# Optimization experiments

Measured on AMD Instinct MI355X. Metric: run time of the kernel, lower is better.

Reference implementation:

```python
import jax, jax.numpy as jnp
import numpy as np

N_LAYER = 2


def setup_inputs() -> dict:
    key = jax.random.key(0)
    k1, k2, k3, k4, k5 = jax.random.split(key, 5)
    N, E, D, C = 50000, 800000, 128, 40
    features = jax.random.normal(k1, (N, D), dtype=jnp.float32)
    adj_row = jax.random.randint(k2, (E,), 0, N, dtype=jnp.int32)
    adj_col = jax.random.randint(k3, (E,), 0, N, dtype=jnp.int32)
    adj_values = jax.random.uniform(k4, (E,), dtype=jnp.float32)
    lin = jax.random.normal(k5, (D, C), dtype=jnp.float32) * (1.0 / np.sqrt(D))
    return {"features": features, "adj_row": adj_row, "adj_col": adj_col,
            "adj_values": adj_values, "lin": lin}


def reference(features, adj_row, adj_col, adj_values, lin):
    N = features.shape[0]
    loop = jnp.arange(N, dtype=adj_row.dtype)
    # preprocess_adj: add self-loops, symmetric GCN normalization D^-1/2 (A+I) D^-1/2
    row = jnp.concatenate([adj_row, loop])
    col = jnp.concatenate([adj_col, loop])
    val = jnp.concatenate([adj_values, jnp.ones((N,), features.dtype)])
    deg = jax.ops.segment_sum(val, row, num_segments=N)
    dinv = jnp.where(deg > 0, jax.lax.rsqrt(jnp.maximum(deg, 1e-12)), 0.0)
    nval = dinv[row] * val * dinv[col]  # normalized edge weights [E+N]
    X = features
    layerwise = []
    for _ in range(N_LAYER):  # X = A_hat @ X (SpMM via gather + segment_sum)
        X = jax.ops.segment_sum(nval[:, None] * X[col], row, num_segments=N)
        layerwise.append(X)
    logits = X @ lin  # [N, out_dim]
    return (jax.nn.log_softmax(logits, axis=1), logits, tuple(layerwise))
```

## Files before the change

kernel.cpp:

```cpp
#include <hip/hip_runtime.h>
#include <math.h>

#define D_FEAT 128
#define SCAN_B 256
#define C_MAX  40
#define FIXP   33554432.0f

#define FLAG_AGG (1ull << 32)
#define FLAG_INC (2ull << 32)


__device__ __forceinline__ unsigned bf16_rne(float x) {
    unsigned u = __float_as_uint(x);
    return (u + 0x7fffu + ((u >> 16) & 1u)) >> 16;
}
__device__ __forceinline__ unsigned pack2(float x, float y) {
    return bf16_rne(x) | (bf16_rne(y) << 16);
}
__device__ __forceinline__ float lo_f(unsigned g) { return __uint_as_float(g << 16); }
__device__ __forceinline__ float hi_f(unsigned g) { return __uint_as_float(g & 0xffff0000u); }


__global__ void k_init(unsigned long long* __restrict__ deg64,
                       unsigned* __restrict__ ticket,
                       unsigned long long* __restrict__ chunkState,
                       int N, int nchunks) {
    int i = blockIdx.x * blockDim.x + threadIdx.x;
    if (i < N) deg64[i] = (unsigned long long)(1.0f * FIXP);
    if (i < nchunks) chunkState[i] = 0ull;
    if (i == 0) *ticket = 0u;
}

__global__ void k_deg_hist(const int* __restrict__ row, const float* __restrict__ val,
                           unsigned long long* __restrict__ deg64,
                           int* __restrict__ rank, int E) {
    int e = blockIdx.x * blockDim.x + threadIdx.x;
    if (e >= E) return;
    int r = row[e];
    unsigned long long add = (1ull << 40) |
                             (unsigned long long)(val[e] * FIXP + 0.5f);
    unsigned long long old = atomicAdd(&deg64[r], add);
    rank[e] = (int)(old >> 40);
}


__global__ __launch_bounds__(SCAN_B) void k_scan_all(const unsigned long long* __restrict__ deg64,
                                                     float* __restrict__ dinv,
                                                     int* __restrict__ rowptr,
                                                     int2* __restrict__ csr,
                                                     unsigned* __restrict__ ticket,
                                                     unsigned long long* __restrict__ chunkState,
                                                     int N, int nchunks) {
    __shared__ int s[SCAN_B];
    __shared__ int vc_s, exc_s;
    int t = threadIdx.x;
    if (t == 0) vc_s = (int)atomicAdd(ticket, 1u);
    __syncthreads();
    int vc = vc_s;
    int i = vc * SCAN_B + t;

    int cr = 0, c = 0;
    if (i < N) {
        unsigned long long p = deg64[i];
        cr = (int)(p >> 40);
        float deg = (float)(p & ((1ull << 40) - 1)) * (1.0f / FIXP);
        dinv[i] = rsqrtf(fmaxf(deg, 1e-12f));
        c = (cr + 7) & ~7;
    }
    s[t] = c;
    __syncthreads();
    for (int off = 1; off < SCAN_B; off <<= 1) {
        int add = (t >= off) ? s[t - off] : 0;
        __syncthreads();
        s[t] += add;
        __syncthreads();
    }
    int incl = s[t];
    int blockSum = s[SCAN_B - 1];

    if (t == 0) {
        int exc = 0;
        if (vc == 0) {
            atomicExch(&chunkState[0], FLAG_INC | (unsigned long long)(unsigned)blockSum);
        } else {
            atomicExch(&chunkState[vc], FLAG_AGG | (unsigned long long)(unsigned)blockSum);
            int j = vc - 1;
            int acc = 0;
            for (;;) {
                unsigned long long st;
                do { st = atomicAdd(&chunkState[j], 0ull); } while ((st >> 32) == 0);
                acc += (int)(st & 0xffffffffull);
                if (st & FLAG_INC) break;
                --j;
            }
            exc = acc;
            atomicExch(&chunkState[vc], FLAG_INC | (unsigned long long)(unsigned)(acc + blockSum));
        }
        exc_s = exc;
    }
    __syncthreads();
    int base = exc_s;

    if (i < N) {
        int rp = base + incl - c;
        rowptr[i] = rp;
        for (int k = cr; k < c; ++k) csr[rp + k] = make_int2(0, 0);
    }
    if (vc == nchunks - 1 && t == SCAN_B - 1) rowptr[N] = base + incl;
}

__global__ void k_scatter_convert(const int* __restrict__ row, const int* __restrict__ col,
                                  const float* __restrict__ val, const int* __restrict__ rank,
                                  const int* __restrict__ rowptr, int2* __restrict__ csr,
                                  const float* __restrict__ X, const float* __restrict__ dinv,
                                  unsigned* __restrict__ Xb, int E, int NV) {
    int t = blockIdx.x * blockDim.x + threadIdx.x;
    if (t < E) {
        int r = row[t];
        csr[rowptr[r] + rank[t]] = make_int2(col[t] << 8, __float_as_int(val[t]));
    } else {
        int u = t - E;
        if (u < NV) {
            float w = dinv[u >> 4];
            float4 a = ((const float4*)X)[u * 2];
            float4 b = ((const float4*)X)[u * 2 + 1];
            uint4 o;
            o.x = pack2(w * a.x, w * a.y); o.y = pack2(w * a.z, w * a.w);
            o.z = pack2(w * b.x, w * b.y); o.w = pack2(w * b.z, w * b.w);
            ((uint4*)Xb)[u] = o;
        }
    }
}

__global__ void k_scatter(const int* __restrict__ row, const int* __restrict__ col,
                          const float* __restrict__ val, const int* __restrict__ rank,
                          const int* __restrict__ rowptr, int2* __restrict__ csr, int E) {
    int e = blockIdx.x * blockDim.x + threadIdx.x;
    if (e >= E) return;
    int r = row[e];
    csr[rowptr[r] + rank[e]] = make_int2(col[e] << 8, __float_as_int(val[e]));
}


__device__ __forceinline__ float2 spmm_row_bf16(const int* __restrict__ rowptr,
                                                const int2* __restrict__ csr,
                                                const char* __restrict__ XbB,
                                                int rowi, int lane) {
    const unsigned lane4 = (unsigned)lane << 2;
    unsigned gs = *(const unsigned*)(XbB + ((unsigned)rowi << 8) + lane4);
    float2 a0 = make_float2(lo_f(gs), hi_f(gs));
    float2 a1 = make_float2(0.f, 0.f), a2 = make_float2(0.f, 0.f), a3 = make_float2(0.f, 0.f);
    int e  = rowptr[rowi];
    int e1 = rowptr[rowi + 1];

    for (; e + 16 <= e1; e += 16) {
        const int4* cp = (const int4*)(csr + e);
        int4 q0 = cp[0], q1 = cp[1], q2 = cp[2], q3 = cp[3];
        int4 q4 = cp[4], q5 = cp[5], q6 = cp[6], q7 = cp[7];
        unsigned g0 = *(const unsigned*)(XbB + (unsigned)q0.x + lane4);
        unsigned g1 = *(const unsigned*)(XbB + (unsigned)q0.z + lane4);
        unsigned g2 = *(const unsigned*)(XbB + (unsigned)q1.x + lane4);
        unsigned g3 = *(const unsigned*)(XbB + (unsigned)q1.z + lane4);
        unsigned g4 = *(const unsigned*)(XbB + (unsigned)q2.x + lane4);
        unsigned g5 = *(const unsigned*)(XbB + (unsigned)q2.z + lane4);
        unsigned g6 = *(const unsigned*)(XbB + (unsigned)q3.x + lane4);
        unsigned g7 = *(const unsigned*)(XbB + (unsigned)q3.z + lane4);
        unsigned g8 = *(const unsigned*)(XbB + (unsigned)q4.x + lane4);
        unsigned g9 = *(const unsigned*)(XbB + (unsigned)q4.z + lane4);
        unsigned ga = *(const unsigned*)(XbB + (unsigned)q5.x + lane4);
        unsigned gb = *(const unsigned*)(XbB + (unsigned)q5.z + lane4);
        unsigned gc = *(const unsigned*)(XbB + (unsigned)q6.x + lane4);
        unsigned gd = *(const unsigned*)(XbB + (unsigned)q6.z + lane4);
        unsigned ge = *(const unsigned*)(XbB + (unsigned)q7.x + lane4);
        unsigned gf = *(const unsigned*)(XbB + (unsigned)q7.z + lane4);
        float w0 = __int_as_float(q0.y), w1 = __int_as_float(q0.w);
        float w2 = __int_as_float(q1.y), w3 = __int_as_float(q1.w);
        float w4 = __int_as_float(q2.y), w5 = __int_as_float(q2.w);
        float w6 = __int_as_float(q3.y), w7 = __int_as_float(q3.w);
        float w8 = __int_as_float(q4.y), w9 = __int_as_float(q4.w);
        float wa = __int_as_float(q5.y), wb = __int_as_float(q5.w);
        float wc = __int_as_float(q6.y), wd = __int_as_float(q6.w);
        float we = __int_as_float(q7.y), wf = __int_as_float(q7.w);
        a0.x += w0 * lo_f(g0); a0.y += w0 * hi_f(g0);
        a1.x += w1 * lo_f(g1); a1.y += w1 * hi_f(g1);
        a2.x += w2 * lo_f(g2); a2.y += w2 * hi_f(g2);
        a3.x += w3 * lo_f(g3); a3.y += w3 * hi_f(g3);
        a0.x += w4 * lo_f(g4); a0.y += w4 * hi_f(g4);
        a1.x += w5 * lo_f(g5); a1.y += w5 * hi_f(g5);
        a2.x += w6 * lo_f(g6); a2.y += w6 * hi_f(g6);
        a3.x += w7 * lo_f(g7); a3.y += w7 * hi_f(g7);
        a0.x += w8 * lo_f(g8); a0.y += w8 * hi_f(g8);
        a1.x += w9 * lo_f(g9); a1.y += w9 * hi_f(g9);
        a2.x += wa * lo_f(ga); a2.y += wa * hi_f(ga);
        a3.x += wb * lo_f(gb); a3.y += wb * hi_f(gb);
        a0.x += wc * lo_f(gc); a0.y += wc * hi_f(gc);
        a1.x += wd * lo_f(gd); a1.y += wd * hi_f(gd);
        a2.x += we * lo_f(ge); a2.y += we * hi_f(ge);
        a3.x += wf * lo_f(gf); a3.y += wf * hi_f(gf);
    }
    if (e < e1) {
        const int4* cp = (const int4*)(csr + e);
        int4 q0 = cp[0], q1 = cp[1], q2 = cp[2], q3 = cp[3];
        unsigned g0 = *(const unsigned*)(XbB + (unsigned)q0.x + lane4);
        unsigned g1 = *(const unsigned*)(XbB + (unsigned)q0.z + lane4);
        unsigned g2 = *(const unsigned*)(XbB + (unsigned)q1.x + lane4);
        unsigned g3 = *(const unsigned*)(XbB + (unsigned)q1.z + lane4);
        unsigned g4 = *(const unsigned*)(XbB + (unsigned)q2.x + lane4);
        unsigned g5 = *(const unsigned*)(XbB + (unsigned)q2.z + lane4);
        unsigned g6 = *(const unsigned*)(XbB + (unsigned)q3.x + lane4);
        unsigned g7 = *(const unsigned*)(XbB + (unsigned)q3.z + lane4);
        float w0 = __int_as_float(q0.y), w1 = __int_as_float(q0.w);
        float w2 = __int_as_float(q1.y), w3 = __int_as_float(q1.w);
        float w4 = __int_as_float(q2.y), w5 = __int_as_float(q2.w);
        float w6 = __int_as_float(q3.y), w7 = __int_as_float(q3.w);
        a0.x += w0 * lo_f(g0); a0.y += w0 * hi_f(g0);
        a1.x += w1 * lo_f(g1); a1.y += w1 * hi_f(g1);
        a2.x += w2 * lo_f(g2); a2.y += w2 * hi_f(g2);
        a3.x += w3 * lo_f(g3); a3.y += w3 * hi_f(g3);
        a0.x += w4 * lo_f(g4); a0.y += w4 * hi_f(g4);
        a1.x += w5 * lo_f(g5); a1.y += w5 * hi_f(g5);
        a2.x += w6 * lo_f(g6); a2.y += w6 * hi_f(g6);
        a3.x += w7 * lo_f(g7); a3.y += w7 * hi_f(g7);
    }
    float2 acc;
    acc.x = (a0.x + a1.x) + (a2.x + a3.x);
    acc.y = (a0.y + a1.y) + (a2.y + a3.y);
    return acc;
}


__global__ __launch_bounds__(256) void k_spmm_l1(const int* __restrict__ rowptr,
                                                 const int2* __restrict__ csr,
                                                 const float* __restrict__ dinv,
                                                 const unsigned* __restrict__ Xb,
                                                 float* __restrict__ Xout,
                                                 unsigned* __restrict__ XbOut, int N) {
    int lane = threadIdx.x & 63;
    int wid  = threadIdx.x >> 6;
    int rowi = blockIdx.x * 4 + wid;
    if (rowi >= N) return;
    float2 acc = spmm_row_bf16(rowptr, csr, (const char*)Xb, rowi, lane);
    float dr = dinv[rowi];
    float2 x1 = make_float2(dr * acc.x, dr * acc.y);
    ((float2*)Xout)[(size_t)rowi * 64 + lane] = x1;
    XbOut[((unsigned)rowi << 6) | lane] = pack2(dr * x1.x, dr * x1.y);
}

__global__ __launch_bounds__(256) void k_spmm_l2_head(const int* __restrict__ rowptr,
                                                      const int2* __restrict__ csr,
                                                      const float* __restrict__ dinv,
                                                      const unsigned* __restrict__ Xb,
                                                      float* __restrict__ Xout,
                                                      const float* __restrict__ lin,
                                                      float* __restrict__ lsm,
                                                      float* __restrict__ logits,
                                                      int N, int C) {
    __shared__ float lin_s[D_FEAT * C_MAX];
    __shared__ float xs[4][D_FEAT];
    int lane = threadIdx.x & 63;
    int wid  = threadIdx.x >> 6;
    int rowi = blockIdx.x * 4 + wid;

    for (int i = threadIdx.x; i < D_FEAT * C; i += 256) lin_s[i] = lin[i];

    if (rowi < N) {
        float2 acc = spmm_row_bf16(rowptr, csr, (const char*)Xb, rowi, lane);
        float dr = dinv[rowi];
        float2 x2 = make_float2(dr * acc.x, dr * acc.y);
        ((float2*)Xout)[(size_t)rowi * 64 + lane] = x2;
        xs[wid][2 * lane]     = x2.x;
        xs[wid][2 * lane + 1] = x2.y;
    }
    __syncthreads();
    if (rowi >= N) return;

    float a = 0.0f;
    if (lane < C) {
#pragma unroll 8
        for (int d = 0; d < D_FEAT; ++d)
            a += xs[wid][d] * lin_s[d * C + lane];
    }
    float m = (lane < C) ? a : -INFINITY;
    for (int off = 32; off; off >>= 1) m = fmaxf(m, __shfl_xor(m, off));
    float ev = (lane < C) ? __expf(a - m) : 0.0f;
    float s = ev;
    for (int off = 32; off; off >>= 1) s += __shfl_xor(s, off);
    float lse = m + logf(s);
    if (lane < C) {
        logits[(size_t)rowi * C + lane] = a;
        lsm[(size_t)rowi * C + lane]    = a - lse;
    }
}


__global__ __launch_bounds__(256) void k_spmm_f32(const int* __restrict__ rowptr,
                                                  const int2* __restrict__ csr,
                                                  const float* __restrict__ dinv,
                                                  const float* __restrict__ Xin,
                                                  float* __restrict__ Xout, int N) {
    int lane = threadIdx.x & 63;
    int wid  = threadIdx.x >> 6;
    int rowi = blockIdx.x * 4 + wid;
    if (rowi >= N) return;
    const float2* Xin2 = (const float2*)Xin;
    float dr = dinv[rowi];
    float2 v0 = Xin2[(size_t)rowi * 64 + lane];
    float2 a0 = make_float2(dr * v0.x, dr * v0.y);
    float2 a1 = make_float2(0.f, 0.f);
    int e  = rowptr[rowi];
    int e1 = rowptr[rowi + 1];
    for (; e < e1; e += 2) {
        int2 q0 = csr[e], q1 = csr[e + 1];
        unsigned c0 = (unsigned)q0.x >> 8, c1 = (unsigned)q1.x >> 8;
        float w0 = __int_as_float(q0.y) * dinv[c0];
        float w1 = __int_as_float(q1.y) * dinv[c1];
        float2 g0 = Xin2[(size_t)c0 * 64 + lane];
        float2 g1 = Xin2[(size_t)c1 * 64 + lane];
        a0.x += w0 * g0.x; a0.y += w0 * g0.y;
        a1.x += w1 * g1.x; a1.y += w1 * g1.y;
    }
    float2 acc = make_float2(dr * (a0.x + a1.x), dr * (a0.y + a1.y));
    ((float2*)Xout)[(size_t)rowi * 64 + lane] = acc;
}

__global__ __launch_bounds__(256) void k_head(const float* __restrict__ X,
                                              const float* __restrict__ lin,
                                              float* __restrict__ lsm,
                                              float* __restrict__ logits,
                                              int N, int C) {
    __shared__ float xs[4][D_FEAT];
    int lane = threadIdx.x & 63;
    int wid  = threadIdx.x >> 6;
    int node = blockIdx.x * 4 + wid;
    if (node < N) {
        xs[wid][lane]      = X[(size_t)node * D_FEAT + lane];
        xs[wid][lane + 64] = X[(size_t)node * D_FEAT + 64 + lane];
    }
    __syncthreads();
    if (node >= N) return;

    float acc = 0.0f;
    if (lane < C) {
        for (int d = 0; d < D_FEAT; ++d)
            acc += xs[wid][d] * lin[d * C + lane];
    }
    float m = (lane < C) ? acc : -INFINITY;
    for (int off = 32; off; off >>= 1) m = fmaxf(m, __shfl_xor(m, off));
    float ev = (lane < C) ? __expf(acc - m) : 0.0f;
    float s = ev;
    for (int off = 32; off; off >>= 1) s += __shfl_xor(s, off);
    float lse = m + logf(s);
    if (lane < C) {
        logits[(size_t)node * C + lane] = acc;
        lsm[(size_t)node * C + lane]    = acc - lse;
    }
}


extern "C" void kernel_launch(void* const* d_in, const int* in_sizes, int n_in,
                              void* d_out, int out_size, void* d_ws, size_t ws_size,
                              hipStream_t stream) {
    const float* features = (const float*)d_in[0];
    const int*   adj_row  = (const int*)d_in[1];
    const int*   adj_col  = (const int*)d_in[2];
    const float* adj_val  = (const float*)d_in[3];
    const float* lin      = (const float*)d_in[4];

    const int N = in_sizes[0] / D_FEAT;
    const int E = in_sizes[1];
    const int C = in_sizes[4] / D_FEAT;
    const int csrTot = E + 8 * N;
    const int nchunks = (N + SCAN_B - 1) / SCAN_B;

    float* out = (float*)d_out;
    const size_t NC = (size_t)N * C;
    const size_t ND = (size_t)N * D_FEAT;
    float* lsm    = out;
    float* logits = out + NC;
    float* X1     = out + 2 * NC;
    float* X2     = out + 2 * NC + ND;

    char* wp = (char*)d_ws;
    auto alloc = [&](size_t bytes) { char* p = wp; wp += (bytes + 15) & ~(size_t)15; return p; };
    unsigned long long* deg64      = (unsigned long long*)alloc((size_t)N * 8);
    float*              dinv       = (float*)alloc((size_t)N * 4);
    int*                rowptr     = (int*)alloc((size_t)(N + 1) * 4);
    unsigned*           ticket     = (unsigned*)alloc(16);
    unsigned long long* chunkState = (unsigned long long*)alloc((size_t)nchunks * 8);
    int*                rank       = (int*)alloc((size_t)E * 4);
    int2*               csr        = (int2*)alloc((size_t)csrTot * 8);
    unsigned*           Xb0        = (unsigned*)alloc((size_t)N * (D_FEAT / 2) * 4);
    unsigned*           Xb1        = (unsigned*)alloc((size_t)N * (D_FEAT / 2) * 4);

    const bool bf16_ok = ((size_t)(wp - (char*)d_ws) <= ws_size) && (C <= C_MAX);

    const int B = 256;

    k_init<<<(N + B - 1) / B, B, 0, stream>>>(deg64, ticket, chunkState, N, nchunks);
    k_deg_hist<<<(E + B - 1) / B, B, 0, stream>>>(adj_row, adj_val, deg64, rank, E);
    k_scan_all<<<nchunks, SCAN_B, 0, stream>>>(deg64, dinv, rowptr, csr,
                                               ticket, chunkState, N, nchunks);

    if (bf16_ok) {
        const int NV = N * (D_FEAT / 8);
        k_scatter_convert<<<(E + NV + B - 1) / B, B, 0, stream>>>(adj_row, adj_col, adj_val,
                                                                  rank, rowptr, csr,
                                                                  features, dinv, Xb0, E, NV);
        int spmmBlocks = (N + 3) / 4;
        k_spmm_l1<<<spmmBlocks, 256, 0, stream>>>(rowptr, csr, dinv, Xb0, X1, Xb1, N);
        k_spmm_l2_head<<<spmmBlocks, 256, 0, stream>>>(rowptr, csr, dinv, Xb1, X2,
                                                       lin, lsm, logits, N, C);
    } else {
        k_scatter<<<(E + B - 1) / B, B, 0, stream>>>(adj_row, adj_col, adj_val, rank,
                                                     rowptr, csr, E);
        int spmmBlocks = (N + 3) / 4;
        k_spmm_f32<<<spmmBlocks, 256, 0, stream>>>(rowptr, csr, dinv, features, X1, N);
        k_spmm_f32<<<spmmBlocks, 256, 0, stream>>>(rowptr, csr, dinv, X1, X2, N);
        k_head<<<(N + 3) / 4, 256, 0, stream>>>(X2, lin, lsm, logits, N, C);
    }
}
```

Before: 181.0 us.

## Split CSR into SoA offset/weight arrays and software-pipeline the SpMM gathers

Replaces the interleaved int2 CSR entries with separate offset and weight arrays so gather addresses load as contiguous int4 vectors. Rewrites the bf16 SpMM row loop as a two-stage software pipeline over 8-edge batches, issuing the next batch's gathers before accumulating the current one, with sched_barrier to hold that order. The goal is more memory-level parallelism and better latency hiding. In exchange it raises register pressure and pads the CSR allocation so prefetched offsets can read past the row end.

```diff
diff --git a/kernel.cpp b/kernel.cpp
--- a/kernel.cpp
+++ b/kernel.cpp
@@ -47,7 +47,8 @@
 __global__ __launch_bounds__(SCAN_B) void k_scan_all(const unsigned long long* __restrict__ deg64,
                                                      float* __restrict__ dinv,
                                                      int* __restrict__ rowptr,
-                                                     int2* __restrict__ csr,
+                                                     int* __restrict__ csrOff,
+                                                     float* __restrict__ csrW,
                                                      unsigned* __restrict__ ticket,
                                                      unsigned long long* __restrict__ chunkState,
                                                      int N, int nchunks) {
@@ -104,20 +105,23 @@
     if (i < N) {
         int rp = base + incl - c;
         rowptr[i] = rp;
-        for (int k = cr; k < c; ++k) csr[rp + k] = make_int2(0, 0);
+        for (int k = cr; k < c; ++k) { csrOff[rp + k] = 0; csrW[rp + k] = 0.0f; }
     }
     if (vc == nchunks - 1 && t == SCAN_B - 1) rowptr[N] = base + incl;
 }
 
 __global__ void k_scatter_convert(const int* __restrict__ row, const int* __restrict__ col,
                                   const float* __restrict__ val, const int* __restrict__ rank,
-                                  const int* __restrict__ rowptr, int2* __restrict__ csr,
+                                  const int* __restrict__ rowptr,
+                                  int* __restrict__ csrOff, float* __restrict__ csrW,
                                   const float* __restrict__ X, const float* __restrict__ dinv,
                                   unsigned* __restrict__ Xb, int E, int NV) {
     int t = blockIdx.x * blockDim.x + threadIdx.x;
     if (t < E) {
         int r = row[t];
-        csr[rowptr[r] + rank[t]] = make_int2(col[t] << 8, __float_as_int(val[t]));
+        int pos = rowptr[r] + rank[t];
+        csrOff[pos] = col[t] << 8;
+        csrW[pos]   = val[t];
     } else {
         int u = t - E;
         if (u < NV) {
@@ -134,16 +138,48 @@
 
 __global__ void k_scatter(const int* __restrict__ row, const int* __restrict__ col,
                           const float* __restrict__ val, const int* __restrict__ rank,
-                          const int* __restrict__ rowptr, int2* __restrict__ csr, int E) {
+                          const int* __restrict__ rowptr,
+                          int* __restrict__ csrOff, float* __restrict__ csrW, int E) {
     int e = blockIdx.x * blockDim.x + threadIdx.x;
     if (e >= E) return;
     int r = row[e];
-    csr[rowptr[r] + rank[e]] = make_int2(col[e] << 8, __float_as_int(val[e]));
-}
-
+    int pos = rowptr[r] + rank[e];
+    csrOff[pos] = col[e] << 8;
+    csrW[pos]   = val[e];
+}
+
+
+struct G8 { unsigned g0, g1, g2, g3, g4, g5, g6, g7; };
+
+__device__ __forceinline__ G8 gather8(const char* __restrict__ XbB,
+                                      int4 o0, int4 o1, unsigned lane4) {
+    G8 r;
+    r.g0 = *(const unsigned*)(XbB + (unsigned)o0.x + lane4);
+    r.g1 = *(const unsigned*)(XbB + (unsigned)o0.y + lane4);
+    r.g2 = *(const unsigned*)(XbB + (unsigned)o0.z + lane4);
+    r.g3 = *(const unsigned*)(XbB + (unsigned)o0.w + lane4);
+    r.g4 = *(const unsigned*)(XbB + (unsigned)o1.x + lane4);
+    r.g5 = *(const unsigned*)(XbB + (unsigned)o1.y + lane4);
+    r.g6 = *(const unsigned*)(XbB + (unsigned)o1.z + lane4);
+    r.g7 = *(const unsigned*)(XbB + (unsigned)o1.w + lane4);
+    return r;
+}
+
+__device__ __forceinline__ void acc8(const G8& g, float4 w0, float4 w1,
+                                     float2& a0, float2& a1, float2& a2, float2& a3) {
+    a0.x += w0.x * lo_f(g.g0); a0.y += w0.x * hi_f(g.g0);
+    a1.x += w0.y * lo_f(g.g1); a1.y += w0.y * hi_f(g.g1);
+    a2.x += w0.z * lo_f(g.g2); a2.y += w0.z * hi_f(g.g2);
+    a3.x += w0.w * lo_f(g.g3); a3.y += w0.w * hi_f(g.g3);
+    a0.x += w1.x * lo_f(g.g4); a0.y += w1.x * hi_f(g.g4);
+    a1.x += w1.y * lo_f(g.g5); a1.y += w1.y * hi_f(g.g5);
+    a2.x += w1.z * lo_f(g.g6); a2.y += w1.z * hi_f(g.g6);
+    a3.x += w1.w * lo_f(g.g7); a3.y += w1.w * hi_f(g.g7);
+}
 
 __device__ __forceinline__ float2 spmm_row_bf16(const int* __restrict__ rowptr,
-                                                const int2* __restrict__ csr,
+                                                const int* __restrict__ csrOff,
+                                                const float* __restrict__ csrW,
                                                 const char* __restrict__ XbB,
                                                 int rowi, int lane) {
     const unsigned lane4 = (unsigned)lane << 2;
@@ -152,75 +188,39 @@
     float2 a1 = make_float2(0.f, 0.f), a2 = make_float2(0.f, 0.f), a3 = make_float2(0.f, 0.f);
     int e  = rowptr[rowi];
     int e1 = rowptr[rowi + 1];
-
-    for (; e + 16 <= e1; e += 16) {
-        const int4* cp = (const int4*)(csr + e);
-        int4 q0 = cp[0], q1 = cp[1], q2 = cp[2], q3 = cp[3];
-        int4 q4 = cp[4], q5 = cp[5], q6 = cp[6], q7 = cp[7];
-        unsigned g0 = *(const unsigned*)(XbB + (unsigned)q0.x + lane4);
-        unsigned g1 = *(const unsigned*)(XbB + (unsigned)q0.z + lane4);
-        unsigned g2 = *(const unsigned*)(XbB + (unsigned)q1.x + lane4);
-        unsigned g3 = *(const unsigned*)(XbB + (unsigned)q1.z + lane4);
-        unsigned g4 = *(const unsigned*)(XbB + (unsigned)q2.x + lane4);
-        unsigned g5 = *(const unsigned*)(XbB + (unsigned)q2.z + lane4);
-        unsigned g6 = *(const unsigned*)(XbB + (unsigned)q3.x + lane4);
-        unsigned g7 = *(const unsigned*)(XbB + (unsigned)q3.z + lane4);
-        unsigned g8 = *(const unsigned*)(XbB + (unsigned)q4.x + lane4);
-        unsigned g9 = *(const unsigned*)(XbB + (unsigned)q4.z + lane4);
-        unsigned ga = *(const unsigned*)(XbB + (unsigned)q5.x + lane4);
-        unsigned gb = *(const unsigned*)(XbB + (unsigned)q5.z + lane4);
-        unsigned gc = *(const unsigned*)(XbB + (unsigned)q6.x + lane4);
-        unsigned gd = *(const unsigned*)(XbB + (unsigned)q6.z + lane4);
-        unsigned ge = *(const unsigned*)(XbB + (unsigned)q7.x + lane4);
-        unsigned gf = *(const unsigned*)(XbB + (unsigned)q7.z + lane4);
-        float w0 = __int_as_float(q0.y), w1 = __int_as_float(q0.w);
-        float w2 = __int_as_float(q1.y), w3 = __int_as_float(q1.w);
-        float w4 = __int_as_float(q2.y), w5 = __int_as_float(q2.w);
-        float w6 = __int_as_float(q3.y), w7 = __int_as_float(q3.w);
-        float w8 = __int_as_float(q4.y), w9 = __int_as_float(q4.w);
-        float wa = __int_as_float(q5.y), wb = __int_as_float(q5.w);
-        float wc = __int_as_float(q6.y), wd = __int_as_float(q6.w);
-        float we = __int_as_float(q7.y), wf = __int_as_float(q7.w);
-        a0.x += w0 * lo_f(g0); a0.y += w0 * hi_f(g0);
-        a1.x += w1 * lo_f(g1); a1.y += w1 * hi_f(g1);
-        a2.x += w2 * lo_f(g2); a2.y += w2 * hi_f(g2);
-        a3.x += w3 * lo_f(g3); a3.y += w3 * hi_f(g3);
-        a0.x += w4 * lo_f(g4); a0.y += w4 * hi_f(g4);
-        a1.x += w5 * lo_f(g5); a1.y += w5 * hi_f(g5);
-        a2.x += w6 * lo_f(g6); a2.y += w6 * hi_f(g6);
-        a3.x += w7 * lo_f(g7); a3.y += w7 * hi_f(g7);
-        a0.x += w8 * lo_f(g8); a0.y += w8 * hi_f(g8);
-        a1.x += w9 * lo_f(g9); a1.y += w9 * hi_f(g9);
-        a2.x += wa * lo_f(ga); a2.y += wa * hi_f(ga);
-        a3.x += wb * lo_f(gb); a3.y += wb * hi_f(gb);
-        a0.x += wc * lo_f(gc); a0.y += wc * hi_f(gc);
-        a1.x += wd * lo_f(gd); a1.y += wd * hi_f(gd);
-        a2.x += we * lo_f(ge); a2.y += we * hi_f(ge);
-        a3.x += wf * lo_f(gf); a3.y += wf * hi_f(gf);
-    }
-    if (e < e1) {
-        const int4* cp = (const int4*)(csr + e);
-        int4 q0 = cp[0], q1 = cp[1], q2 = cp[2], q3 = cp[3];
-        unsigned g0 = *(const unsigned*)(XbB + (unsigned)q0.x + lane4);
-        unsigned g1 = *(const unsigned*)(XbB + (unsigned)q0.z + lane4);
-        unsigned g2 = *(const unsigned*)(XbB + (unsigned)q1.x + lane4);
-        unsigned g3 = *(const unsigned*)(XbB + (unsigned)q1.z + lane4);
-        unsigned g4 = *(const unsigned*)(XbB + (unsigned)q2.x + lane4);
-        unsigned g5 = *(const unsigned*)(XbB + (unsigned)q2.z + lane4);
-        unsigned g6 = *(const unsigned*)(XbB + (unsigned)q3.x + lane4);
-        unsigned g7 = *(const unsigned*)(XbB + (unsigned)q3.z + lane4);
-        float w0 = __int_as_float(q0.y), w1 = __int_as_float(q0.w);
-        float w2 = __int_as_float(q1.y), w3 = __int_as_float(q1.w);
-        float w4 = __int_as_float(q2.y), w5 = __int_as_float(q2.w);
-        float w6 = __int_as_float(q3.y), w7 = __int_as_float(q3.w);
-        a0.x += w0 * lo_f(g0); a0.y += w0 * hi_f(g0);
-        a1.x += w1 * lo_f(g1); a1.y += w1 * hi_f(g1);
-        a2.x += w2 * lo_f(g2); a2.y += w2 * hi_f(g2);
-        a3.x += w3 * lo_f(g3); a3.y += w3 * hi_f(g3);
-        a0.x += w4 * lo_f(g4); a0.y += w4 * hi_f(g4);
-        a1.x += w5 * lo_f(g5); a1.y += w5 * hi_f(g5);
-        a2.x += w6 * lo_f(g6); a2.y += w6 * hi_f(g6);
-        a3.x += w7 * lo_f(g7); a3.y += w7 * hi_f(g7);
+    int nb = (e1 - e) >> 3;
+
+    if (nb > 0) {
+        const int4*   op = (const int4*)(csrOff + e);
+        const float4* wp = (const float4*)(csrW + e);
+
+        int4 oA0 = op[0], oA1 = op[1];
+        G8 gA = gather8(XbB, oA0, oA1, lane4);
+        float4 wA0 = wp[0], wA1 = wp[1];
+        int4 oB0 = op[2], oB1 = op[3];
+
+        int k = 1;
+        for (; k + 1 < nb; k += 2) {
+            int4 nA0 = op[2 * k + 2], nA1 = op[2 * k + 3];
+            G8 gB = gather8(XbB, oB0, oB1, lane4);
+            float4 wB0 = wp[2 * k], wB1 = wp[2 * k + 1];
+            __builtin_amdgcn_sched_barrier(0);
+            acc8(gA, wA0, wA1, a0, a1, a2, a3);
+            oB0 = op[2 * k + 4]; oB1 = op[2 * k + 5];
+            gA = gather8(XbB, nA0, nA1, lane4);
+            wA0 = wp[2 * k + 2]; wA1 = wp[2 * k + 3];
+            __builtin_amdgcn_sched_barrier(0);
+            acc8(gB, wB0, wB1, a0, a1, a2, a3);
+        }
+        if (k < nb) {
+            G8 gB = gather8(XbB, oB0, oB1, lane4);
+            float4 wB0 = wp[2 * k], wB1 = wp[2 * k + 1];
+            __builtin_amdgcn_sched_barrier(0);
+            acc8(gA, wA0, wA1, a0, a1, a2, a3);
+            acc8(gB, wB0, wB1, a0, a1, a2, a3);
+        } else {
+            acc8(gA, wA0, wA1, a0, a1, a2, a3);
+        }
     }
     float2 acc;
     acc.x = (a0.x + a1.x) + (a2.x + a3.x);
@@ -230,7 +230,8 @@
 
 
 __global__ __launch_bounds__(256) void k_spmm_l1(const int* __restrict__ rowptr,
-                                                 const int2* __restrict__ csr,
+                                                 const int* __restrict__ csrOff,
+                                                 const float* __restrict__ csrW,
                                                  const float* __restrict__ dinv,
                                                  const unsigned* __restrict__ Xb,
                                                  float* __restrict__ Xout,
@@ -239,7 +240,7 @@
     int wid  = threadIdx.x >> 6;
     int rowi = blockIdx.x * 4 + wid;
     if (rowi >= N) return;
-    float2 acc = spmm_row_bf16(rowptr, csr, (const char*)Xb, rowi, lane);
+    float2 acc = spmm_row_bf16(rowptr, csrOff, csrW, (const char*)Xb, rowi, lane);
     float dr = dinv[rowi];
     float2 x1 = make_float2(dr * acc.x, dr * acc.y);
     ((float2*)Xout)[(size_t)rowi * 64 + lane] = x1;
@@ -247,7 +248,8 @@
 }
 
 __global__ __launch_bounds__(256) void k_spmm_l2_head(const int* __restrict__ rowptr,
-                                                      const int2* __restrict__ csr,
+                                                      const int* __restrict__ csrOff,
+                                                      const float* __restrict__ csrW,
                                                       const float* __restrict__ dinv,
                                                       const unsigned* __restrict__ Xb,
                                                       float* __restrict__ Xout,
@@ -264,7 +266,7 @@
     for (int i = threadIdx.x; i < D_FEAT * C; i += 256) lin_s[i] = lin[i];
 
     if (rowi < N) {
-        float2 acc = spmm_row_bf16(rowptr, csr, (const char*)Xb, rowi, lane);
+        float2 acc = spmm_row_bf16(rowptr, csrOff, csrW, (const char*)Xb, rowi, lane);
         float dr = dinv[rowi];
         float2 x2 = make_float2(dr * acc.x, dr * acc.y);
         ((float2*)Xout)[(size_t)rowi * 64 + lane] = x2;
@@ -294,7 +296,8 @@
 
 
 __global__ __launch_bounds__(256) void k_spmm_f32(const int* __restrict__ rowptr,
-                                                  const int2* __restrict__ csr,
+                                                  const int* __restrict__ csrOff,
+                                                  const float* __restrict__ csrW,
                                                   const float* __restrict__ dinv,
                                                   const float* __restrict__ Xin,
                                                   float* __restrict__ Xout, int N) {
@@ -310,10 +313,9 @@
     int e  = rowptr[rowi];
     int e1 = rowptr[rowi + 1];
     for (; e < e1; e += 2) {
-        int2 q0 = csr[e], q1 = csr[e + 1];
-        unsigned c0 = (unsigned)q0.x >> 8, c1 = (unsigned)q1.x >> 8;
-        float w0 = __int_as_float(q0.y) * dinv[c0];
-        float w1 = __int_as_float(q1.y) * dinv[c1];
+        unsigned c0 = (unsigned)csrOff[e] >> 8, c1 = (unsigned)csrOff[e + 1] >> 8;
+        float w0 = csrW[e] * dinv[c0];
+        float w1 = csrW[e + 1] * dinv[c1];
         float2 g0 = Xin2[(size_t)c0 * 64 + lane];
         float2 g1 = Xin2[(size_t)c1 * 64 + lane];
         a0.x += w0 * g0.x; a0.y += w0 * g0.y;
@@ -369,7 +371,7 @@
     const int N = in_sizes[0] / D_FEAT;
     const int E = in_sizes[1];
     const int C = in_sizes[4] / D_FEAT;
-    const int csrTot = E + 8 * N;
+    const int csrTot = E + 8 * N + 16;
     const int nchunks = (N + SCAN_B - 1) / SCAN_B;
 
     float* out = (float*)d_out;
@@ -388,7 +390,8 @@
     unsigned*           ticket     = (unsigned*)alloc(16);
     unsigned long long* chunkState = (unsigned long long*)alloc((size_t)nchunks * 8);
     int*                rank       = (int*)alloc((size_t)E * 4);
-    int2*               csr        = (int2*)alloc((size_t)csrTot * 8);
+    int*                csrOff     = (int*)alloc((size_t)csrTot * 4);
+    float*              csrW       = (float*)alloc((size_t)csrTot * 4);
     unsigned*           Xb0        = (unsigned*)alloc((size_t)N * (D_FEAT / 2) * 4);
     unsigned*           Xb1        = (unsigned*)alloc((size_t)N * (D_FEAT / 2) * 4);
 
@@ -398,24 +401,24 @@
 
     k_init<<<(N + B - 1) / B, B, 0, stream>>>(deg64, ticket, chunkState, N, nchunks);
     k_deg_hist<<<(E + B - 1) / B, B, 0, stream>>>(adj_row, adj_val, deg64, rank, E);
-    k_scan_all<<<nchunks, SCAN_B, 0, stream>>>(deg64, dinv, rowptr, csr,
+    k_scan_all<<<nchunks, SCAN_B, 0, stream>>>(deg64, dinv, rowptr, csrOff, csrW,
                                                ticket, chunkState, N, nchunks);
 
     if (bf16_ok) {
         const int NV = N * (D_FEAT / 8);
         k_scatter_convert<<<(E + NV + B - 1) / B, B, 0, stream>>>(adj_row, adj_col, adj_val,
-                                                                  rank, rowptr, csr,
+                                                                  rank, rowptr, csrOff, csrW,
                                                                   features, dinv, Xb0, E, NV);
         int spmmBlocks = (N + 3) / 4;
-        k_spmm_l1<<<spmmBlocks, 256, 0, stream>>>(rowptr, csr, dinv, Xb0, X1, Xb1, N);
-        k_spmm_l2_head<<<spmmBlocks, 256, 0, stream>>>(rowptr, csr, dinv, Xb1, X2,
+        k_spmm_l1<<<spmmBlocks, 256, 0, stream>>>(rowptr, csrOff, csrW, dinv, Xb0, X1, Xb1, N);
+        k_spmm_l2_head<<<spmmBlocks, 256, 0, stream>>>(rowptr, csrOff, csrW, dinv, Xb1, X2,
                                                        lin, lsm, logits, N, C);
     } else {
         k_scatter<<<(E + B - 1) / B, B, 0, stream>>>(adj_row, adj_col, adj_val, rank,
-                                                     rowptr, csr, E);
+                                                     rowptr, csrOff, csrW, E);
         int spmmBlocks = (N + 3) / 4;
-        k_spmm_f32<<<spmmBlocks, 256, 0, stream>>>(rowptr, csr, dinv, features, X1, N);
-        k_spmm_f32<<<spmmBlocks, 256, 0, stream>>>(rowptr, csr, dinv, X1, X2, N);
+        k_spmm_f32<<<spmmBlocks, 256, 0, stream>>>(rowptr, csrOff, csrW, dinv, features, X1, N);
+        k_spmm_f32<<<spmmBlocks, 256, 0, stream>>>(rowptr, csrOff, csrW, dinv, X1, X2, N);
         k_head<<<(N + 3) / 4, 256, 0, stream>>>(X2, lin, lsm, logits, N, C);
     }
 }
```

Result: slower. 218.3 us (+20.6%).
